# Kernel optimization log

Measured on AMD Instinct MI355X. Metric: run time of the kernel, lower is better.

The kernel has to match this reference:

```python
import jax, jax.numpy as jnp
import numpy as np

H = 16          # num_heads
RMS_EPS = 1.1920928955078125e-07  # torch.finfo(float32).eps (F.rms_norm default)
NORM_EPS = 1e-12                  # F.normalize default eps


def _rms_norm(t):
    # F.rms_norm without weight: t / sqrt(mean(t^2) + eps)
    ms = jnp.mean(t * t, axis=-1, keepdims=True)
    return t * jax.lax.rsqrt(ms + RMS_EPS)


def setup_inputs() -> dict:
    key = jax.random.key(0)
    k1, k2, k3 = jax.random.split(key, 3)
    B, N, C = 2, 2048, 1024
    x = jax.random.normal(k1, (B, N, C), dtype=jnp.float32)
    # nn.Linear weights are (out_features, in_features); scale like kaiming-uniform-ish
    w_qkv = jax.random.normal(k2, (3 * C, C), dtype=jnp.float32) * (C ** -0.5)
    w_proj = jax.random.normal(k3, (C, C), dtype=jnp.float32) * (C ** -0.5)
    return {"x": x, "w_qkv": w_qkv, "w_proj": w_proj}


def reference(x, w_qkv, w_proj):
    B, N, C = x.shape
    D = C // H
    scale = D ** -0.5
    qkv = x @ w_qkv.T                                  # (B,N,3C)
    qkv = qkv.reshape(B, N, 3, H, D)
    q = qkv[:, :, 0].transpose(0, 2, 1, 3)             # (B,H,N,D)
    k = qkv[:, :, 1].transpose(0, 2, 1, 3)
    v = qkv[:, :, 2].transpose(0, 2, 1, 3)
    q = _rms_norm(q)
    k = _rms_norm(k)
    attn = jnp.einsum('bhnd,bhmd->bhnm', q, k) * scale  # (B,H,N,N)
    attn = jax.nn.softmax(attn, axis=-1)
    y = jnp.einsum('bhnm,bhmd->bhnd', attn, v)          # (B,H,N,D)
    # xsa: subtract projection of y onto normalized v
    vnorm = jnp.linalg.norm(v, axis=-1, keepdims=True)
    Vn = v / jnp.maximum(vnorm, NORM_EPS)
    y = y - jnp.sum(y * Vn, axis=-1, keepdims=True) * Vn
    out = y.transpose(0, 2, 1, 3).reshape(B, N, C)
    return out @ w_proj.T
```

## Files before the change

### kernel.cpp

```cpp
#include <hip/hip_runtime.h>
#include <hip/hip_bf16.h>
#include <cstdint>

#define RMS_EPS 1.1920928955078125e-07f

typedef __bf16 bf16;
typedef __attribute__((ext_vector_type(8))) __bf16 bf16x8;
typedef __attribute__((ext_vector_type(4))) __bf16 bf16x4;
typedef __attribute__((ext_vector_type(4))) float f32x4;
typedef __attribute__((ext_vector_type(16))) float f32x16;
typedef unsigned int u32;
typedef __attribute__((ext_vector_type(4))) u32 u32x4;

__device__ __forceinline__ void gload16(const bf16* g, bf16* l) {
  __builtin_amdgcn_global_load_lds(
      (__attribute__((address_space(1))) void*)(g),
      (__attribute__((address_space(3))) void*)(l), 16, 0, 0);
}

__device__ __forceinline__ float fexp2(float x) {
#if __has_builtin(__builtin_amdgcn_exp2f)
  return __builtin_amdgcn_exp2f(x);
#else
  return exp2f(x);
#endif
}

__device__ __forceinline__ u32 pack2(float a, float b) {
  unsigned short xa = __builtin_bit_cast(unsigned short, (bf16)a);
  unsigned short xb = __builtin_bit_cast(unsigned short, (bf16)b);
  return (u32)xa | ((u32)xb << 16);
}

__global__ __launch_bounds__(256) void cvt3_kernel(
    const float* __restrict__ x, const float* __restrict__ wq, const float* __restrict__ wp,
    bf16* __restrict__ xo, bf16* __restrict__ wqo, bf16* __restrict__ wpo) {
  int i = blockIdx.x * 256 + threadIdx.x;
  const float* s; bf16* d; int off;
  if (i < 524288) { s = x; d = xo; off = i; }
  else if (i < 917504) { s = wq; d = wqo; off = i - 524288; }
  else { s = wp; d = wpo; off = i - 917504; }
  const float4* s4 = (const float4*)s;
  float4 a = s4[off * 2], b = s4[off * 2 + 1];
  bf16x8 o;
  o[0] = (bf16)a.x; o[1] = (bf16)a.y; o[2] = (bf16)a.z; o[3] = (bf16)a.w;
  o[4] = (bf16)b.x; o[5] = (bf16)b.y; o[6] = (bf16)b.z; o[7] = (bf16)b.w;
  *(bf16x8*)(d + off * 8) = o;
}

template <int MODE>
__global__ __launch_bounds__(256, 2) void gemm_bt(
    const bf16* __restrict__ A, const bf16* __restrict__ B,
    float* __restrict__ Cout, int Ncols,
    bf16* __restrict__ Qb, bf16* __restrict__ Kb, bf16* __restrict__ Vb,
    float* __restrict__ vninv) {
  __shared__ bf16 As[128 * 64];
  __shared__ bf16 Bs[128 * 64];
  const int tid = threadIdx.x;
  const int wave = tid >> 6, lane = tid & 63;
  const int l15 = lane & 15, g = lane >> 4;
  const int nwg = gridDim.x * gridDim.y;
  const int wg0 = blockIdx.y * gridDim.x + blockIdx.x;
  const int wg = (wg0 & 7) * (nwg >> 3) + (wg0 >> 3);
  const int m0 = (wg / gridDim.x) * 128, n0 = (wg % gridDim.x) * 128;
  const int wr = wave >> 1, wc = wave & 1;

  f32x4 acc[4][4] = {};

  for (int k0 = 0; k0 < 1024; k0 += 64) {
    __syncthreads();
#pragma unroll
    for (int i = 0; i < 4; ++i) {
      const int gid = (i * 4 + wave) * 64 + lane;
      const int row = gid >> 3, gk = gid & 7;
      const int srcoff = k0 + ((gk ^ (row & 7)) << 3);
      gload16(A + (m0 + row) * 1024 + srcoff, As + (i * 4 + wave) * 512);
      gload16(B + (n0 + row) * 1024 + srcoff, Bs + (i * 4 + wave) * 512);
    }
    __syncthreads();
#pragma unroll
    for (int kc = 0; kc < 2; ++kc) {
      bf16x8 af[4], bfb[4];
#pragma unroll
      for (int mi = 0; mi < 4; ++mi) {
        const int row = wr * 64 + mi * 16 + l15;
        af[mi] = *(const bf16x8*)&As[row * 64 + (((kc * 4 + g) ^ (l15 & 7)) << 3)];
      }
#pragma unroll
      for (int ni = 0; ni < 4; ++ni) {
        const int row = wc * 64 + ni * 16 + l15;
        bfb[ni] = *(const bf16x8*)&Bs[row * 64 + (((kc * 4 + g) ^ (l15 & 7)) << 3)];
      }
#pragma unroll
      for (int mi = 0; mi < 4; ++mi)
#pragma unroll
        for (int ni = 0; ni < 4; ++ni)
          acc[mi][ni] = __builtin_amdgcn_mfma_f32_16x16x32_bf16(af[mi], bfb[ni], acc[mi][ni], 0, 0, 0);
    }
  }

  if (MODE == 0) {
#pragma unroll
    for (int mi = 0; mi < 4; ++mi) {
      const int mrow = m0 + wr * 64 + mi * 16 + g * 4;
#pragma unroll
      for (int r = 0; r < 4; ++r) {
        float* cp = Cout + (long)(mrow + r) * Ncols + n0 + wc * 64 + l15;
#pragma unroll
        for (int ni = 0; ni < 4; ++ni) cp[ni * 16] = acc[mi][ni][r];
      }
    }
  } else {
    const int ncol = n0 + wc * 64;
    const int which = ncol >> 10;
    const int h = (ncol >> 6) & 15;
#pragma unroll
    for (int mi = 0; mi < 4; ++mi) {
#pragma unroll
      for (int r = 0; r < 4; ++r) {
        float ss = 0.f;
#pragma unroll
        for (int ni = 0; ni < 4; ++ni) ss += acc[mi][ni][r] * acc[mi][ni][r];
        ss += __shfl_xor(ss, 1); ss += __shfl_xor(ss, 2);
        ss += __shfl_xor(ss, 4); ss += __shfl_xor(ss, 8);
        const int m = m0 + wr * 64 + mi * 16 + g * 4 + r;
        const int b = m >> 11, nseq = m & 2047;
        const long base = ((long)(b * 16 + h) * 2048 + nseq) * 64 + l15;
        if (which == 0) {
          const float sc = rsqrtf(ss * (1.0f / 64) + RMS_EPS) * (0.125f * 1.44269504088896340736f);
#pragma unroll
          for (int ni = 0; ni < 4; ++ni) Qb[base + ni * 16] = (bf16)(acc[mi][ni][r] * sc);
        } else if (which == 1) {
          const float sc = rsqrtf(ss * (1.0f / 64) + RMS_EPS);
#pragma unroll
          for (int ni = 0; ni < 4; ++ni) Kb[base + ni * 16] = (bf16)(acc[mi][ni][r] * sc);
        } else {
#pragma unroll
          for (int ni = 0; ni < 4; ++ni) Vb[base + ni * 16] = (bf16)acc[mi][ni][r];
          if (l15 == 0) vninv[(b * 16 + h) * 2048 + nseq] = 1.0f / fmaxf(sqrtf(ss), 1e-12f);
        }
      }
    }
  }
}

__global__ __launch_bounds__(256, 2) void attn_kernel(
    const bf16* __restrict__ Qb, const bf16* __restrict__ Kb, const bf16* __restrict__ Vb,
    const float* __restrict__ vninv, bf16* __restrict__ Yb) {
  __shared__ bf16 Ks[2][64 * 64];
  __shared__ bf16 Vt[2][64 * 64];

  const int tid = threadIdx.x;
  const int wq = tid >> 6;
  const int lane = tid & 63;
  const int l31 = lane & 31, hi = lane >> 5;
  const int wg = (blockIdx.x & 7) * (gridDim.x >> 3) + (blockIdx.x >> 3);
  const int bh = wg >> 4, qb = wg & 15;
  const int b = bh >> 4, h = bh & 15;
  const long off = (long)bh * (2048 * 64);
  const bf16* Qp = Qb + off;
  const bf16* Kp = Kb + off;
  const bf16* Vp = Vb + off;
  const int qrow = qb * 128 + wq * 32 + l31;

  bf16x8 qf[4];
#pragma unroll
  for (int kc = 0; kc < 4; ++kc)
    qf[kc] = *(const bf16x8*)&Qp[qrow * 64 + kc * 16 + hi * 8];

  f32x16 o[2] = {};
  float mrun = -__builtin_inff();
  float lrun = 0.f;

  const int kj = lane >> 3, kgk = lane & 7;
#pragma unroll
  for (int i = 0; i < 2; ++i) {
    const int chunk = i * 4 + wq;
    const int j = chunk * 8 + kj;
    gload16(Kp + j * 64 + ((kgk ^ (j & 7)) << 3), &Ks[0][chunk * 512]);
  }
#pragma unroll
  for (int i = 0; i < 2; ++i) {
    const int gid = i * 256 + tid;
    const int j = gid >> 3, gk = gid & 7, jg = gid >> 6;
    bf16x8 v8 = *(const bf16x8*)&Vp[j * 64 + gk * 8];
#pragma unroll
    for (int e = 0; e < 8; ++e)
      Vt[0][(gk * 8 + e) * 64 + ((jg ^ gk ^ e) << 3) + (j & 7)] = v8[e];
  }
  __syncthreads();

  int cur = 0;
  for (int kv0 = 0; kv0 < 2048; kv0 += 64) {
    const bool pf = (kv0 + 64) < 2048;
    bf16x8 v8[2];
    if (pf) {
#pragma unroll
      for (int i = 0; i < 2; ++i) {
        const int chunk = i * 4 + wq;
        const int j = chunk * 8 + kj;
        gload16(Kp + (kv0 + 64 + j) * 64 + ((kgk ^ (j & 7)) << 3), &Ks[cur ^ 1][chunk * 512]);
      }
#pragma unroll
      for (int i = 0; i < 2; ++i) {
        const int gid = i * 256 + tid;
        v8[i] = *(const bf16x8*)&Vp[(kv0 + 64 + (gid >> 3)) * 64 + (gid & 7) * 8];
      }
    }
    const bf16* ks = &Ks[cur][0];
    const bf16* vt = &Vt[cur][0];

    f32x16 sv[2] = {};
    __builtin_amdgcn_s_setprio(1);
#pragma unroll
    for (int jt = 0; jt < 2; ++jt) {
      const int j = jt * 32 + l31;
#pragma unroll
      for (int kc = 0; kc < 4; ++kc) {
        bf16x8 kf = *(const bf16x8*)&ks[j * 64 + (((2 * kc + hi) ^ (j & 7)) << 3)];
        sv[jt] = __builtin_amdgcn_mfma_f32_32x32x16_bf16(kf, qf[kc], sv[jt], 0, 0, 0);
      }
    }
    __builtin_amdgcn_s_setprio(0);

    float mx[16];
#pragma unroll
    for (int r = 0; r < 16; ++r) mx[r] = fmaxf(sv[0][r], sv[1][r]);
#pragma unroll
    for (int s2 = 8; s2 > 0; s2 >>= 1)
#pragma unroll
      for (int r = 0; r < s2; ++r) mx[r] = fmaxf(mx[r], mx[r + s2]);
    float pmax = fmaxf(mx[0], __shfl_xor(mx[0], 32));

    if (!__all(pmax <= mrun + 8.f)) {
      const float mn = fmaxf(mrun, pmax);
      const float al = fexp2(mrun - mn);
      mrun = mn;
      lrun *= al;
#pragma unroll
      for (int dt = 0; dt < 2; ++dt)
#pragma unroll
        for (int r = 0; r < 16; ++r) o[dt][r] *= al;
    }

#pragma unroll
    for (int jt = 0; jt < 2; ++jt)
#pragma unroll
      for (int r = 0; r < 16; ++r) sv[jt][r] = fexp2(sv[jt][r] - mrun);
    float sm[16];
#pragma unroll
    for (int r = 0; r < 16; ++r) sm[r] = sv[0][r] + sv[1][r];
#pragma unroll
    for (int s2 = 8; s2 > 0; s2 >>= 1)
#pragma unroll
      for (int r = 0; r < s2; ++r) sm[r] += sm[r + s2];
    lrun += sm[0] + __shfl_xor(sm[0], 32);

    u32 w[2][8], pw[2][8];
#pragma unroll
    for (int jt = 0; jt < 2; ++jt)
#pragma unroll
      for (int i = 0; i < 8; ++i) {
        w[jt][i] = pack2(sv[jt][2 * i], sv[jt][2 * i + 1]);
        pw[jt][i] = __shfl_xor(w[jt][i], 32);
      }
    bf16x8 pafr[4];
#pragma unroll
    for (int kc = 0; kc < 4; ++kc) {
      const int c = kc & 1, jt = kc >> 1;
      u32x4 pv;
      pv[0] = hi ? pw[jt][4 * c + 2] : w[jt][4 * c];
      pv[1] = hi ? pw[jt][4 * c + 3] : w[jt][4 * c + 1];
      pv[2] = hi ? w[jt][4 * c + 2] : pw[jt][4 * c];
      pv[3] = hi ? w[jt][4 * c + 3] : pw[jt][4 * c + 1];
      pafr[kc] = __builtin_bit_cast(bf16x8, pv);
    }

    __builtin_amdgcn_s_setprio(1);
#pragma unroll
    for (int dt = 0; dt < 2; ++dt) {
      const int d = dt * 32 + l31;
      const int key = ((d >> 3) ^ d) & 7;
#pragma unroll
      for (int kc = 0; kc < 4; ++kc) {
        bf16x8 vf = *(const bf16x8*)&vt[d * 64 + (((2 * kc + hi) ^ key) << 3)];
        o[dt] = __builtin_amdgcn_mfma_f32_32x32x16_bf16(vf, pafr[kc], o[dt], 0, 0, 0);
      }
    }
    __builtin_amdgcn_s_setprio(0);

    if (pf) {
#pragma unroll
      for (int i = 0; i < 2; ++i) {
        const int gid = i * 256 + tid;
        const int j = gid >> 3, gk = gid & 7, jg = gid >> 6;
#pragma unroll
        for (int e = 0; e < 8; ++e)
          Vt[cur ^ 1][(gk * 8 + e) * 64 + ((jg ^ gk ^ e) << 3) + (j & 7)] = v8[i][e];
      }
    }
    __syncthreads();
    cur ^= 1;
  }

  const float linv = 1.f / lrun;
  const float vni = vninv[bh * 2048 + qrow];
  const float cvn = vni * vni;
  float yv[2][16], vvf[2][16];
  float t = 0.f;
#pragma unroll
  for (int dt = 0; dt < 2; ++dt)
#pragma unroll
    for (int rr = 0; rr < 4; ++rr) {
      bf16x4 v4 = *(const bf16x4*)&Vp[qrow * 64 + dt * 32 + rr * 8 + hi * 4];
#pragma unroll
      for (int e = 0; e < 4; ++e) {
        const int r = rr * 4 + e;
        const float y = o[dt][r] * linv;
        const float vx = (float)v4[e];
        yv[dt][r] = y; vvf[dt][r] = vx;
        t += y * vx;
      }
    }
  t += __shfl_xor(t, 32);
  const float coef = t * cvn;
  bf16* yp = Yb + ((long)b * 2048 + qrow) * 1024 + h * 64;
#pragma unroll
  for (int dt = 0; dt < 2; ++dt)
#pragma unroll
    for (int rr = 0; rr < 4; ++rr) {
      bf16x4 y4;
#pragma unroll
      for (int e = 0; e < 4; ++e) {
        const int r = rr * 4 + e;
        y4[e] = (bf16)(yv[dt][r] - coef * vvf[dt][r]);
      }
      *(bf16x4*)&yp[dt * 32 + rr * 8 + hi * 4] = y4;
    }
}

extern "C" void kernel_launch(void* const* d_in, const int* in_sizes, int n_in,
                              void* d_out, int out_size, void* d_ws, size_t ws_size,
                              hipStream_t stream) {
  (void)in_sizes; (void)n_in; (void)out_size; (void)ws_size;
  const float* x = (const float*)d_in[0];
  const float* w_qkv = (const float*)d_in[1];
  const float* w_proj = (const float*)d_in[2];
  float* out = (float*)d_out;
  char* ws = (char*)d_ws;

  bf16* xb     = (bf16*)(ws);
  bf16* wqkvb  = (bf16*)(ws + 8388608);
  bf16* wprojb = (bf16*)(ws + 14680064);
  bf16* Qb     = (bf16*)(ws + 16777216);
  bf16* Kb     = (bf16*)(ws + 25165824);
  bf16* Vb     = (bf16*)(ws + 33554432);
  float* vninv = (float*)(ws + 41943040);
  bf16* Yb     = (bf16*)(ws + 42467328);

  cvt3_kernel<<<4096, 256, 0, stream>>>(x, w_qkv, w_proj, xb, wqkvb, wprojb);

  gemm_bt<1><<<dim3(24, 32), 256, 0, stream>>>(xb, wqkvb, nullptr, 3072,
                                               Qb, Kb, Vb, vninv);
  attn_kernel<<<512, 256, 0, stream>>>(Qb, Kb, Vb, vninv, Yb);
  gemm_bt<0><<<dim3(8, 32), 256, 0, stream>>>(Yb, wprojb, out, 1024,
                                              nullptr, nullptr, nullptr, nullptr);
}
```

Before: 139.7 us.

## Split attention KV range across two wave groups and merge partial softmax

After: 142.9 us. 2.3% more time.

```diff
diff --git a/kernel.cpp b/kernel.cpp
--- a/kernel.cpp
+++ b/kernel.cpp
@@ -144,14 +144,23 @@
   }
 }
 
-__global__ __launch_bounds__(256, 2) void attn_kernel(
+struct ShMem {
+  union {
+    struct { bf16 Ks[2][2][4096]; bf16 Vt[2][2][4096]; } st;
+    struct { float Oex[4][64][32]; float2 mlex[4][64]; } mg;
+  };
+};
+
+__global__ __launch_bounds__(512, 4) void attn_kernel(
     const bf16* __restrict__ Qb, const bf16* __restrict__ Kb, const bf16* __restrict__ Vb,
     const float* __restrict__ vninv, bf16* __restrict__ Yb) {
-  __shared__ bf16 Ks[2][64 * 64];
-  __shared__ bf16 Vt[2][64 * 64];
+  __shared__ ShMem sh;
 
   const int tid = threadIdx.x;
   const int wq = tid >> 6;
+  const int half = wq >> 2;
+  const int wqh = wq & 3;
+  const int tidh = tid & 255;
   const int lane = tid & 63;
   const int l31 = lane & 31, hi = lane >> 5;
   const int wg = (blockIdx.x & 7) * (gridDim.x >> 3) + (blockIdx.x >> 3);
@@ -161,7 +170,8 @@
   const bf16* Qp = Qb + off;
   const bf16* Kp = Kb + off;
   const bf16* Vp = Vb + off;
-  const int qrow = qb * 128 + wq * 32 + l31;
+  const int qrow = qb * 128 + wqh * 32 + l31;
+  const int kvbase = half * 1024;
 
   bf16x8 qf[4];
 #pragma unroll
@@ -175,40 +185,42 @@
   const int kj = lane >> 3, kgk = lane & 7;
 #pragma unroll
   for (int i = 0; i < 2; ++i) {
-    const int chunk = i * 4 + wq;
+    const int chunk = i * 4 + wqh;
     const int j = chunk * 8 + kj;
-    gload16(Kp + j * 64 + ((kgk ^ (j & 7)) << 3), &Ks[0][chunk * 512]);
+    gload16(Kp + (kvbase + j) * 64 + ((kgk ^ (j & 7)) << 3), &sh.st.Ks[half][0][chunk * 512]);
   }
 #pragma unroll
   for (int i = 0; i < 2; ++i) {
-    const int gid = i * 256 + tid;
+    const int gid = i * 256 + tidh;
     const int j = gid >> 3, gk = gid & 7, jg = gid >> 6;
-    bf16x8 v8 = *(const bf16x8*)&Vp[j * 64 + gk * 8];
+    bf16x8 v8 = *(const bf16x8*)&Vp[(kvbase + j) * 64 + gk * 8];
 #pragma unroll
     for (int e = 0; e < 8; ++e)
-      Vt[0][(gk * 8 + e) * 64 + ((jg ^ gk ^ e) << 3) + (j & 7)] = v8[e];
+      sh.st.Vt[half][0][(gk * 8 + e) * 64 + ((jg ^ gk ^ e) << 3) + (j & 7)] = v8[e];
   }
   __syncthreads();
 
   int cur = 0;
-  for (int kv0 = 0; kv0 < 2048; kv0 += 64) {
-    const bool pf = (kv0 + 64) < 2048;
+  for (int it = 0; it < 16; ++it) {
+    const int kv0 = kvbase + it * 64;
+    const bool pf = it < 15;
     bf16x8 v8[2];
     if (pf) {
 #pragma unroll
       for (int i = 0; i < 2; ++i) {
-        const int chunk = i * 4 + wq;
+        const int chunk = i * 4 + wqh;
         const int j = chunk * 8 + kj;
-        gload16(Kp + (kv0 + 64 + j) * 64 + ((kgk ^ (j & 7)) << 3), &Ks[cur ^ 1][chunk * 512]);
+        gload16(Kp + (kv0 + 64 + j) * 64 + ((kgk ^ (j & 7)) << 3),
+                &sh.st.Ks[half][cur ^ 1][chunk * 512]);
       }
 #pragma unroll
       for (int i = 0; i < 2; ++i) {
-        const int gid = i * 256 + tid;
+        const int gid = i * 256 + tidh;
         v8[i] = *(const bf16x8*)&Vp[(kv0 + 64 + (gid >> 3)) * 64 + (gid & 7) * 8];
       }
     }
-    const bf16* ks = &Ks[cur][0];
-    const bf16* vt = &Vt[cur][0];
+    const bf16* ks = &sh.st.Ks[half][cur][0];
+    const bf16* vt = &sh.st.Vt[half][cur][0];
 
     f32x16 sv[2] = {};
     __builtin_amdgcn_s_setprio(1);
@@ -292,18 +304,57 @@
     if (pf) {
 #pragma unroll
       for (int i = 0; i < 2; ++i) {
-        const int gid = i * 256 + tid;
+        const int gid = i * 256 + tidh;
         const int j = gid >> 3, gk = gid & 7, jg = gid >> 6;
 #pragma unroll
         for (int e = 0; e < 8; ++e)
-          Vt[cur ^ 1][(gk * 8 + e) * 64 + ((jg ^ gk ^ e) << 3) + (j & 7)] = v8[i][e];
+          sh.st.Vt[half][cur ^ 1][(gk * 8 + e) * 64 + ((jg ^ gk ^ e) << 3) + (j & 7)] = v8[i][e];
       }
     }
     __syncthreads();
     cur ^= 1;
   }
 
-  const float linv = 1.f / lrun;
+  const int slot = wqh * 64 + lane;
+  if (half == 1) {
+    float4* dst = (float4*)&sh.mg.Oex[wqh][lane][0];
+#pragma unroll
+    for (int cchunk = 0; cchunk < 8; ++cchunk) {
+      const int cs = cchunk ^ (slot & 7);
+      float4 v;
+      v.x = o[(cchunk * 4 + 0) >> 4][(cchunk * 4 + 0) & 15];
+      v.y = o[(cchunk * 4 + 1) >> 4][(cchunk * 4 + 1) & 15];
+      v.z = o[(cchunk * 4 + 2) >> 4][(cchunk * 4 + 2) & 15];
+      v.w = o[(cchunk * 4 + 3) >> 4][(cchunk * 4 + 3) & 15];
+      dst[cs] = v;
+    }
+    sh.mg.mlex[wqh][lane] = make_float2(mrun, lrun);
+  }
+  __syncthreads();
+  if (half == 1) return;
+
+  const float2 ml1 = sh.mg.mlex[wqh][lane];
+  const float mtot = fmaxf(mrun, ml1.x);
+  const float a0 = fexp2(mrun - mtot), a1 = fexp2(ml1.x - mtot);
+  const float ltot = lrun * a0 + ml1.y * a1;
+  {
+    const float4* src = (const float4*)&sh.mg.Oex[wqh][lane][0];
+#pragma unroll
+    for (int cchunk = 0; cchunk < 8; ++cchunk) {
+      const int cs = cchunk ^ (slot & 7);
+      const float4 v = src[cs];
+      o[(cchunk * 4 + 0) >> 4][(cchunk * 4 + 0) & 15] =
+          o[(cchunk * 4 + 0) >> 4][(cchunk * 4 + 0) & 15] * a0 + v.x * a1;
+      o[(cchunk * 4 + 1) >> 4][(cchunk * 4 + 1) & 15] =
+          o[(cchunk * 4 + 1) >> 4][(cchunk * 4 + 1) & 15] * a0 + v.y * a1;
+      o[(cchunk * 4 + 2) >> 4][(cchunk * 4 + 2) & 15] =
+          o[(cchunk * 4 + 2) >> 4][(cchunk * 4 + 2) & 15] * a0 + v.z * a1;
+      o[(cchunk * 4 + 3) >> 4][(cchunk * 4 + 3) & 15] =
+          o[(cchunk * 4 + 3) >> 4][(cchunk * 4 + 3) & 15] * a0 + v.w * a1;
+    }
+  }
+
+  const float linv = 1.f / ltot;
   const float vni = vninv[bh * 2048 + qrow];
   const float cvn = vni * vni;
   float yv[2][16], vvf[2][16];
@@ -362,7 +413,7 @@
 
   gemm_bt<1><<<dim3(24, 32), 256, 0, stream>>>(xb, wqkvb, nullptr, 3072,
                                                Qb, Kb, Vb, vninv);
-  attn_kernel<<<512, 256, 0, stream>>>(Qb, Kb, Vb, vninv, Yb);
+  attn_kernel<<<512, 512, 0, stream>>>(Qb, Kb, Vb, vninv, Yb);
   gemm_bt<0><<<dim3(8, 32), 256, 0, stream>>>(Yb, wprojb, out, 1024,
                                               nullptr, nullptr, nullptr, nullptr);
 }
```

## Store V transposed in QKV GEMM epilogue and async-load it in attention

Applied to the files above, without the earlier changes.

Result: no change. 142.3 us (+1.9%).

```diff
diff --git a/kernel.cpp b/kernel.cpp
--- a/kernel.cpp
+++ b/kernel.cpp
@@ -52,7 +52,7 @@
 __global__ __launch_bounds__(256, 2) void gemm_bt(
     const bf16* __restrict__ A, const bf16* __restrict__ B,
     float* __restrict__ Cout, int Ncols,
-    bf16* __restrict__ Qb, bf16* __restrict__ Kb, bf16* __restrict__ Vb,
+    bf16* __restrict__ Qb, bf16* __restrict__ Kb, bf16* __restrict__ VtG,
     float* __restrict__ vninv) {
   __shared__ bf16 As[128 * 64];
   __shared__ bf16 Bs[128 * 64];
@@ -125,7 +125,8 @@
         ss += __shfl_xor(ss, 4); ss += __shfl_xor(ss, 8);
         const int m = m0 + wr * 64 + mi * 16 + g * 4 + r;
         const int b = m >> 11, nseq = m & 2047;
-        const long base = ((long)(b * 16 + h) * 2048 + nseq) * 64 + l15;
+        const int bh = b * 16 + h;
+        const long base = ((long)bh * 2048 + nseq) * 64 + l15;
         if (which == 0) {
           const float sc = rsqrtf(ss * (1.0f / 64) + RMS_EPS) * (0.125f * 1.44269504088896340736f);
 #pragma unroll
@@ -135,9 +136,11 @@
 #pragma unroll
           for (int ni = 0; ni < 4; ++ni) Kb[base + ni * 16] = (bf16)(acc[mi][ni][r] * sc);
         } else {
-#pragma unroll
-          for (int ni = 0; ni < 4; ++ni) Vb[base + ni * 16] = (bf16)acc[mi][ni][r];
-          if (l15 == 0) vninv[(b * 16 + h) * 2048 + nseq] = 1.0f / fmaxf(sqrtf(ss), 1e-12f);
+          const long vbase = (long)bh * 64 * 2048 + nseq;
+#pragma unroll
+          for (int ni = 0; ni < 4; ++ni)
+            VtG[vbase + (long)(ni * 16 + l15) * 2048] = (bf16)acc[mi][ni][r];
+          if (l15 == 0) vninv[bh * 2048 + nseq] = 1.0f / fmaxf(sqrtf(ss), 1e-12f);
         }
       }
     }
@@ -145,7 +148,7 @@
 }
 
 __global__ __launch_bounds__(256, 2) void attn_kernel(
-    const bf16* __restrict__ Qb, const bf16* __restrict__ Kb, const bf16* __restrict__ Vb,
+    const bf16* __restrict__ Qb, const bf16* __restrict__ Kb, const bf16* __restrict__ VtG,
     const float* __restrict__ vninv, bf16* __restrict__ Yb) {
   __shared__ bf16 Ks[2][64 * 64];
   __shared__ bf16 Vt[2][64 * 64];
@@ -160,7 +163,7 @@
   const long off = (long)bh * (2048 * 64);
   const bf16* Qp = Qb + off;
   const bf16* Kp = Kb + off;
-  const bf16* Vp = Vb + off;
+  const bf16* VtP = VtG + (long)bh * 64 * 2048;
   const int qrow = qb * 128 + wq * 32 + l31;
 
   bf16x8 qf[4];
@@ -173,38 +176,32 @@
   float lrun = 0.f;
 
   const int kj = lane >> 3, kgk = lane & 7;
+  int koff[2], voff[2];
 #pragma unroll
   for (int i = 0; i < 2; ++i) {
     const int chunk = i * 4 + wq;
-    const int j = chunk * 8 + kj;
-    gload16(Kp + j * 64 + ((kgk ^ (j & 7)) << 3), &Ks[0][chunk * 512]);
-  }
+    const int row = chunk * 8 + kj;
+    const int sw = (kgk ^ (row & 7)) << 3;
+    koff[i] = row * 64 + sw;
+    voff[i] = row * 2048 + sw;
+  }
+
 #pragma unroll
   for (int i = 0; i < 2; ++i) {
-    const int gid = i * 256 + tid;
-    const int j = gid >> 3, gk = gid & 7, jg = gid >> 6;
-    bf16x8 v8 = *(const bf16x8*)&Vp[j * 64 + gk * 8];
-#pragma unroll
-    for (int e = 0; e < 8; ++e)
-      Vt[0][(gk * 8 + e) * 64 + ((jg ^ gk ^ e) << 3) + (j & 7)] = v8[e];
+    const int chunk = i * 4 + wq;
+    gload16(Kp + koff[i], &Ks[0][chunk * 512]);
+    gload16(VtP + voff[i], &Vt[0][chunk * 512]);
   }
   __syncthreads();
 
   int cur = 0;
   for (int kv0 = 0; kv0 < 2048; kv0 += 64) {
-    const bool pf = (kv0 + 64) < 2048;
-    bf16x8 v8[2];
-    if (pf) {
+    if (kv0 + 64 < 2048) {
 #pragma unroll
       for (int i = 0; i < 2; ++i) {
         const int chunk = i * 4 + wq;
-        const int j = chunk * 8 + kj;
-        gload16(Kp + (kv0 + 64 + j) * 64 + ((kgk ^ (j & 7)) << 3), &Ks[cur ^ 1][chunk * 512]);
-      }
-#pragma unroll
-      for (int i = 0; i < 2; ++i) {
-        const int gid = i * 256 + tid;
-        v8[i] = *(const bf16x8*)&Vp[(kv0 + 64 + (gid >> 3)) * 64 + (gid & 7) * 8];
+        gload16(Kp + (kv0 + 64) * 64 + koff[i], &Ks[cur ^ 1][chunk * 512]);
+        gload16(VtP + (kv0 + 64) + voff[i], &Vt[cur ^ 1][chunk * 512]);
       }
     }
     const bf16* ks = &Ks[cur][0];
@@ -280,25 +277,14 @@
 #pragma unroll
     for (int dt = 0; dt < 2; ++dt) {
       const int d = dt * 32 + l31;
-      const int key = ((d >> 3) ^ d) & 7;
 #pragma unroll
       for (int kc = 0; kc < 4; ++kc) {
-        bf16x8 vf = *(const bf16x8*)&vt[d * 64 + (((2 * kc + hi) ^ key) << 3)];
+        bf16x8 vf = *(const bf16x8*)&vt[d * 64 + (((2 * kc + hi) ^ (l31 & 7)) << 3)];
         o[dt] = __builtin_amdgcn_mfma_f32_32x32x16_bf16(vf, pafr[kc], o[dt], 0, 0, 0);
       }
     }
     __builtin_amdgcn_s_setprio(0);
 
-    if (pf) {
-#pragma unroll
-      for (int i = 0; i < 2; ++i) {
-        const int gid = i * 256 + tid;
-        const int j = gid >> 3, gk = gid & 7, jg = gid >> 6;
-#pragma unroll
-        for (int e = 0; e < 8; ++e)
-          Vt[cur ^ 1][(gk * 8 + e) * 64 + ((jg ^ gk ^ e) << 3) + (j & 7)] = v8[i][e];
-      }
-    }
     __syncthreads();
     cur ^= 1;
   }
@@ -306,18 +292,19 @@
   const float linv = 1.f / lrun;
   const float vni = vninv[bh * 2048 + qrow];
   const float cvn = vni * vni;
+  const bf16* vq = VtP + qrow;
   float yv[2][16], vvf[2][16];
   float t = 0.f;
 #pragma unroll
   for (int dt = 0; dt < 2; ++dt)
 #pragma unroll
     for (int rr = 0; rr < 4; ++rr) {
-      bf16x4 v4 = *(const bf16x4*)&Vp[qrow * 64 + dt * 32 + rr * 8 + hi * 4];
 #pragma unroll
       for (int e = 0; e < 4; ++e) {
         const int r = rr * 4 + e;
+        const int d = e + 8 * rr + 4 * hi + 32 * dt;
         const float y = o[dt][r] * linv;
-        const float vx = (float)v4[e];
+        const float vx = (float)vq[d * 2048];
         yv[dt][r] = y; vvf[dt][r] = vx;
         t += y * vx;
       }
@@ -354,15 +341,15 @@
   bf16* wprojb = (bf16*)(ws + 14680064);
   bf16* Qb     = (bf16*)(ws + 16777216);
   bf16* Kb     = (bf16*)(ws + 25165824);
-  bf16* Vb     = (bf16*)(ws + 33554432);
+  bf16* VtG    = (bf16*)(ws + 33554432);
   float* vninv = (float*)(ws + 41943040);
   bf16* Yb     = (bf16*)(ws + 42467328);
 
   cvt3_kernel<<<4096, 256, 0, stream>>>(x, w_qkv, w_proj, xb, wqkvb, wprojb);
 
   gemm_bt<1><<<dim3(24, 32), 256, 0, stream>>>(xb, wqkvb, nullptr, 3072,
-                                               Qb, Kb, Vb, vninv);
-  attn_kernel<<<512, 256, 0, stream>>>(Qb, Kb, Vb, vninv, Yb);
+                                               Qb, Kb, VtG, vninv);
+  attn_kernel<<<512, 256, 0, stream>>>(Qb, Kb, VtG, vninv, Yb);
   gemm_bt<0><<<dim3(8, 32), 256, 0, stream>>>(Yb, wprojb, out, 1024,
                                               nullptr, nullptr, nullptr, nullptr);
 }
```
